# Kernel tuning notes

Hardware: AMD Instinct MI355X
Metric: run time of the kernel (lower is better)

Reference implementation:

```python
import jax, jax.numpy as jnp
import numpy as np

B, T, C, H = 4, 2048, 2048, 16
DH = C // H  # 128

def setup_inputs() -> dict:
    key = jax.random.key(0)
    ks = jax.random.split(key, 5)
    s_in = 1.0 / np.sqrt(C)
    return {
        "x": jax.random.normal(ks[0], (B, T, C), dtype=jnp.float32),
        "qkv_w": jax.random.uniform(ks[1], (3 * C, C), jnp.float32, -s_in, s_in),
        "qkv_b": jax.random.uniform(ks[2], (3 * C,), jnp.float32, -s_in, s_in),
        "proj_w": jax.random.uniform(ks[3], (C, C), jnp.float32, -s_in, s_in),
        "proj_b": jax.random.uniform(ks[4], (C,), jnp.float32, -s_in, s_in),
    }

def reference(x, qkv_w, qkv_b, proj_w, proj_b):
    b, t, _ = x.shape
    qkv = x @ qkv_w.T + qkv_b                     # [B,T,3C]
    q, k, v = jnp.split(qkv, 3, axis=-1)
    # [B,T,C] -> [B,H,T,Dh]
    q = q.reshape(b, t, H, DH).transpose(0, 2, 1, 3)
    k = k.reshape(b, t, H, DH).transpose(0, 2, 1, 3)
    v = v.reshape(b, t, H, DH).transpose(0, 2, 1, 3)
    scores = jnp.einsum('bhqd,bhkd->bhqk', q, k) / jnp.sqrt(jnp.float32(DH))
    causal = jnp.tril(jnp.ones((t, t), dtype=bool))  # [T,T]
    scores = jnp.where(causal[None, None], scores, jnp.finfo(scores.dtype).min)
    att = jax.nn.softmax(scores, axis=-1)
    out = jnp.einsum('bhqk,bhkd->bhqd', att, v)   # [B,H,T,Dh]
    out = out.transpose(0, 2, 1, 3).reshape(b, t, C)
    return out @ proj_w.T + proj_b
```

## Files before the change

kernel.cpp:

```cpp
#include <hip/hip_runtime.h>
#include <stdint.h>


typedef __attribute__((ext_vector_type(8))) short bf8_t;
typedef __attribute__((ext_vector_type(4))) float f4_t;

__device__ __forceinline__ short f2bf(float f) {
  union { float f; uint32_t u; } x; x.f = f;
  uint32_t r = x.u + 0x7fffu + ((x.u >> 16) & 1u);
  return (short)(r >> 16);
}

#define GLD16(gp, lp) __builtin_amdgcn_global_load_lds( \
    (const __attribute__((address_space(1))) void*)(gp), \
    (__attribute__((address_space(3))) void*)(lp), 16, 0, 0)

__device__ __forceinline__ bf8_t dsr(uint32_t a) {
  bf8_t d;
  asm volatile("ds_read_b128 %0, %1" : "=v"(d) : "v"(a));
  return d;
}

#define QSCALE (0.08838834764831845f * 1.4426950408889634f)

__global__ __launch_bounds__(256) void cast3_f32_bf16(
    const float* __restrict__ a, const float* __restrict__ b,
    const float* __restrict__ c, short* __restrict__ oa,
    short* __restrict__ ob, short* __restrict__ oc,
    int na4, int nb4, int nc4) {
  int i = blockIdx.x * blockDim.x + threadIdx.x;
  const float* src; short* dst; int idx;
  if (i < na4) { src = a; dst = oa; idx = i; }
  else if (i < na4 + nb4) { src = b; dst = ob; idx = i - na4; }
  else if (i < na4 + nb4 + nc4) { src = c; dst = oc; idx = i - na4 - nb4; }
  else return;
  float4 v = ((const float4*)src)[idx];
  short4 o;
  o.x = f2bf(v.x); o.y = f2bf(v.y); o.z = f2bf(v.z); o.w = f2bf(v.w);
  ((short4*)dst)[idx] = o;
}


#define BARR() do { __builtin_amdgcn_s_barrier(); \
                    __builtin_amdgcn_sched_barrier(0); } while (0)
#define WAITDS() do { asm volatile("s_waitcnt lgkmcnt(0)" ::: "memory"); \
                      __builtin_amdgcn_sched_barrier(0); } while (0)
#define SB() __builtin_amdgcn_sched_barrier(0)
#define PR1 __builtin_amdgcn_s_setprio(1)
#define PR0 __builtin_amdgcn_s_setprio(0)

#define STAGE(g, loff) do { \
    GLD16((g) + voff0, ldsc + (loff) + dst0); \
    GLD16((g) + voff1, ldsc + (loff) + 8192 + dst0); } while (0)

#define QUAD(CI, CJ, AF, BF)                                                \
  if (!swapAB) {                                                            \
    _Pragma("unroll") for (int kk = 0; kk < 2; ++kk)                        \
    _Pragma("unroll") for (int i = 0; i < 4; ++i)                           \
    _Pragma("unroll") for (int j = 0; j < 2; ++j)                           \
      acc[(CI) + i][(CJ) + j] = __builtin_amdgcn_mfma_f32_16x16x32_bf16(    \
          AF[i][kk], BF[j][kk], acc[(CI) + i][(CJ) + j], 0, 0, 0);          \
  } else {                                                                  \
    _Pragma("unroll") for (int kk = 0; kk < 2; ++kk)                        \
    _Pragma("unroll") for (int i = 0; i < 4; ++i)                           \
    _Pragma("unroll") for (int j = 0; j < 2; ++j)                           \
      acc[(CI) + i][(CJ) + j] = __builtin_amdgcn_mfma_f32_16x16x32_bf16(    \
          BF[j][kk], AF[i][kk], acc[(CI) + i][(CJ) + j], 0, 0, 0);          \
  }

template <int MODE>
__global__ __launch_bounds__(512, 2) void gemm_bt(
    const short* __restrict__ A, const short* __restrict__ Bw,
    const float* __restrict__ bias, float* __restrict__ Cout,
    short* __restrict__ Qo, short* __restrict__ Ko, short* __restrict__ Vo,
    int M, int N, int K) {
  __shared__ __attribute__((aligned(16))) char lds[131072];
  const int tid = threadIdx.x;
  const int lane = tid & 63, wave = tid >> 6;
  const int quad = lane >> 4, l16 = lane & 15;
  const int wm = wave >> 2, wn = wave & 3;

  const int nwg = gridDim.x;
  const int cpx = nwg >> 3;
  const int bid = blockIdx.x;
  const int swz = (bid & 7) * cpx + (bid >> 3);
  const int nbx = N >> 8;
  const int bm = swz / nbx, bn = swz - bm * nbx;
  const int m0 = bm << 8, n0 = bn << 8;

  const int which = (MODE == 0) ? (n0 >> 11) : -1;
  const bool swapAB = (MODE == 0) && (which == 2);


  f4_t acc[8][4];
  if (!swapAB) {
#pragma unroll
    for (int j = 0; j < 4; ++j) {
      const float b0 = bias[n0 + (j >> 1) * 128 + wn * 32 + (j & 1) * 16 + l16];
      const f4_t bv = {b0, b0, b0, b0};
#pragma unroll
      for (int i = 0; i < 8; ++i) acc[i][j] = bv;
    }
  } else {
#pragma unroll
    for (int j = 0; j < 4; ++j)
#pragma unroll
      for (int r = 0; r < 4; ++r) {
        const float b0 =
            bias[n0 + (j >> 1) * 128 + wn * 32 + (j & 1) * 16 + quad * 4 + r];
#pragma unroll
        for (int i = 0; i < 8; ++i) acc[i][j][r] = b0;
      }
  }

  const char* baseA = (const char*)(A + (size_t)m0 * K);
  const char* baseB = (const char*)(Bw + (size_t)n0 * K);
  const size_t hK = (size_t)K << 8;
  const int r0 = tid >> 3;
  const int lg = (tid & 7) ^ (r0 & 7);
  const uint32_t voff0 = (uint32_t)(r0 * K + lg * 8) * 2u;
  const uint32_t voff1 = voff0 + ((uint32_t)K << 7);
  char* ldsc = (char*)lds;
  const int dst0 = tid * 16;

  const int x7 = l16 & 7;
  const int gx0 = (quad ^ x7) << 4;
  const int gx1 = ((quad | 4) ^ x7) << 4;
  const uint32_t lbase =
      (uint32_t)(uintptr_t)(__attribute__((address_space(3))) char*)lds;
  const uint32_t aAg0 = lbase + wm * 8192 + l16 * 128 + gx0;
  const uint32_t aAg1 = lbase + wm * 8192 + l16 * 128 + gx1;
  const uint32_t bBg0 = lbase + 32768 + wn * 4096 + l16 * 128 + gx0;
  const uint32_t bBg1 = lbase + 32768 + wn * 4096 + l16 * 128 + gx1;

  asm volatile("s_waitcnt vmcnt(0)" ::: "memory");
  SB();

  STAGE(baseA, 0);
  STAGE(baseB, 32768);
  STAGE(baseB + hK, 49152);
  STAGE(baseA + hK, 16384);
  STAGE(baseA + 128, 65536 + 0);
  STAGE(baseB + hK + 128, 65536 + 49152);
  STAGE(baseA + hK + 128, 65536 + 16384);
  asm volatile("s_waitcnt vmcnt(6)" ::: "memory");
  SB();
  __builtin_amdgcn_s_barrier();

  const int NT = K >> 6;
  bf8_t af[4][2], b0f[2][2], b1f[2][2];

#pragma unroll
  for (int i = 0; i < 4; ++i) {
    af[i][0] = dsr(aAg0 + i * 2048);
    af[i][1] = dsr(aAg1 + i * 2048);
  }
#pragma unroll
  for (int j = 0; j < 2; ++j) {
    b0f[j][0] = dsr(bBg0 + j * 2048);
    b0f[j][1] = dsr(bBg1 + j * 2048);
  }

  for (int t = 0; t < NT; ++t) {
    const uint32_t s = (uint32_t)(t & 1) << 16;
    const uint32_t o = s ^ 65536u;
    const size_t c1 = (size_t)(t + 1 < NT ? t + 1 : NT - 1) << 7;
    const size_t c2 = (size_t)(t + 2 < NT ? t + 2 : NT - 1) << 7;
    const uint32_t sA0 = aAg0 + s, sA1 = aAg1 + s;
    const uint32_t sB0 = bBg0 + s, sB1 = bBg1 + s;

    WAITDS();
    STAGE(baseB + c1, (int)o + 32768);
    __builtin_amdgcn_s_barrier();
    SB();
    PR1; QUAD(0, 0, af, b0f); PR0;
    SB();
#pragma unroll
    for (int j = 0; j < 2; ++j) {
      b1f[j][0] = dsr(sB0 + 16384 + j * 2048);
      b1f[j][1] = dsr(sB1 + 16384 + j * 2048);
    }
    BARR();

    WAITDS();
    STAGE(baseA + c2, (int)s + 0);
    __builtin_amdgcn_s_barrier();
    SB();
    PR1; QUAD(0, 2, af, b1f); PR0;
    SB();
#pragma unroll
    for (int i = 0; i < 4; ++i) {
      af[i][0] = dsr(sA0 + 16384 + i * 2048);
      af[i][1] = dsr(sA1 + 16384 + i * 2048);
    }
    BARR();

    WAITDS();
    STAGE(baseB + hK + c2, (int)s + 49152);
    __builtin_amdgcn_s_barrier();
    SB();
    PR1; QUAD(4, 2, af, b1f); PR0;
    BARR();

    STAGE(baseA + hK + c2, (int)s + 16384);
    asm volatile("s_waitcnt vmcnt(6)" ::: "memory");
    SB();
    __builtin_amdgcn_s_barrier();
    SB();
    PR1; QUAD(4, 0, af, b0f); PR0;
    SB();
#pragma unroll
    for (int i = 0; i < 4; ++i) {
      af[i][0] = dsr(o + aAg0 + i * 2048);
      af[i][1] = dsr(o + aAg1 + i * 2048);
    }
#pragma unroll
    for (int j = 0; j < 2; ++j) {
      b0f[j][0] = dsr(o + bBg0 + j * 2048);
      b0f[j][1] = dsr(o + bBg1 + j * 2048);
    }
    BARR();
  }

  asm volatile("s_waitcnt vmcnt(0) lgkmcnt(0)" ::: "memory");
  SB();

  if (MODE == 1) {
#pragma unroll
    for (int i = 0; i < 8; ++i) {
      const int mg = m0 + (i >> 2) * 128 + wm * 64 + (i & 3) * 16 + quad * 4;
#pragma unroll
      for (int r = 0; r < 4; ++r) {
        const size_t mrow = (size_t)(mg + r) * N;
#pragma unroll
        for (int j = 0; j < 4; ++j) {
          const int ng = n0 + (j >> 1) * 128 + wn * 32 + (j & 1) * 16 + l16;
          Cout[mrow + ng] = acc[i][j][r];
        }
      }
    }
  } else if (!swapAB) {
    short* dst = (which == 0) ? Qo : Ko;
    const float sc = (which == 0) ? QSCALE : 1.0f;
#pragma unroll
    for (int i = 0; i < 8; ++i) {
      const int mg = m0 + (i >> 2) * 128 + wm * 64 + (i & 3) * 16 + quad * 4;
#pragma unroll
      for (int r = 0; r < 4; ++r) {
        const int m = mg + r;
        const int b = m >> 11, tt = m & 2047;
#pragma unroll
        for (int j = 0; j < 4; ++j) {
          const int ng = n0 + (j >> 1) * 128 + wn * 32 + (j & 1) * 16 + l16;
          const int h = (ng & 2047) >> 7, d = ng & 127;
          dst[((size_t)((b * 16 + h) * 2048 + tt)) * 128 + d] =
              f2bf(acc[i][j][r] * sc);
        }
      }
    }
  } else {
#pragma unroll
    for (int i = 0; i < 8; ++i) {
      const int mg = m0 + (i >> 2) * 128 + wm * 64 + (i & 3) * 16 + l16;
      const int b = mg >> 11, tt = mg & 2047;
#pragma unroll
      for (int j = 0; j < 4; ++j) {
        const int nb = n0 + (j >> 1) * 128 + wn * 32 + (j & 1) * 16 + quad * 4;
#pragma unroll
        for (int r = 0; r < 4; ++r) {
          const int ng = nb + r;
          const int h = (ng & 2047) >> 7, d = ng & 127;
          Vo[((size_t)((b * 16 + h) * 128 + d)) * 2048 + tt] =
              f2bf(acc[i][j][r]);
        }
      }
    }
  }
}

__global__ __launch_bounds__(256) void attn_fwd(
    const short* __restrict__ Qg, const short* __restrict__ Kg,
    const short* __restrict__ Vtg, short* __restrict__ Og) {
  __shared__ __attribute__((aligned(16))) short lK[64 * 128];
  __shared__ __attribute__((aligned(16))) short lV[128 * 64];
  __shared__ __attribute__((aligned(16))) short lP[4 * 2048];
  const int tid = threadIdx.x;
  const int lane = tid & 63, wave = tid >> 6;
  const int quad = lane >> 4, l16 = lane & 15;
  const int bid = blockIdx.x;
  const int bh = ((bid & 7) << 3) | ((bid >> 3) & 7);
  const int p = bid >> 6;
  const size_t baseK = (size_t)bh * (2048 * 128);
  const size_t baseV = (size_t)bh * (128 * 2048);
  const int x7 = l16 & 7;
  const int b = bh >> 4, h = bh & 15;
  short* lPw = lP + wave * 2048;
  const f4_t fz = {0.f, 0.f, 0.f, 0.f};

  uint32_t vK[4], vV[4];
#pragma unroll
  for (int r = 0; r < 4; ++r) {
    const int off = tid * 16 + r * 4096;
    const int rowK = off >> 8;
    const int lcK = ((off >> 4) & 15) ^ (rowK & 7);
    vK[r] = (uint32_t)(rowK * 128 + lcK * 8) * 2u;
    const int dV = off >> 7;
    const int lcV = ((off >> 4) & 7) ^ (dV & 7);
    vV[r] = (uint32_t)(dV * 2048 + lcV * 8) * 2u;
  }

  for (int job = 0; job < 2; ++job) {
    const int bx = job ? (15 - p) : p;
    const int q0 = bx * 128;
    const int qw = q0 + wave * 32;

    bf8_t qf[2][4];
#pragma unroll
    for (int m = 0; m < 2; ++m)
#pragma unroll
      for (int dc = 0; dc < 4; ++dc)
        qf[m][dc] = *(const bf8_t*)(Qg + baseK + (size_t)(qw + m * 16 + l16) * 128 + dc * 32 + quad * 8);

    f4_t o[2][8];
#pragma unroll
    for (int m = 0; m < 2; ++m)
#pragma unroll
      for (int n = 0; n < 8; ++n) o[m][n] = fz;
    float lsum[2][4];
#pragma unroll
    for (int m = 0; m < 2; ++m)
#pragma unroll
      for (int r = 0; r < 4; ++r) lsum[m][r] = 0.f;

    const char* kbase = (const char*)(Kg + baseK);
    const char* vbase = (const char*)(Vtg + baseV);
    const int ktmax = 2 * bx + 1;
    for (int kt = 0; kt <= ktmax; ++kt) {
      const int k0 = kt * 64;
      __syncthreads();
#pragma unroll
      for (int r = 0; r < 4; ++r) {
        const int off = tid * 16 + r * 4096;
        GLD16(kbase + vK[r], (char*)lK + off);
        GLD16(vbase + vV[r], (char*)lV + off);
      }
      kbase += 16384;
      vbase += 128;
      __syncthreads();
      if (k0 >= qw + 32) continue;

      f4_t s[2][4];
#pragma unroll
      for (int m = 0; m < 2; ++m)
#pragma unroll
        for (int g = 0; g < 4; ++g) s[m][g] = fz;
#pragma unroll
      for (int g = 0; g < 4; ++g)
#pragma unroll
        for (int dc = 0; dc < 4; ++dc) {
          bf8_t kf = *(const bf8_t*)(lK + (g * 16 + l16) * 128 + (((dc * 4 + quad) ^ x7) << 3));
          s[0][g] = __builtin_amdgcn_mfma_f32_16x16x32_bf16(qf[0][dc], kf, s[0][g], 0, 0, 0);
          s[1][g] = __builtin_amdgcn_mfma_f32_16x16x32_bf16(qf[1][dc], kf, s[1][g], 0, 0, 0);
        }
#pragma unroll
      for (int m = 0; m < 2; ++m) {
        const int qbase = qw + m * 16;
        const bool nomask = (k0 + 63 <= qbase);
#pragma unroll
        for (int g = 0; g < 4; ++g) {
          const int key = k0 + g * 16 + l16;
#pragma unroll
          for (int r = 0; r < 4; ++r) {
            float pv = exp2f(s[m][g][r]);
            if (!nomask && key > qbase + quad * 4 + r) pv = 0.f;
            lsum[m][r] += pv;
            const int row = quad * 4 + r;
            lPw[m * 1024 + row * 64 + (((g * 2 + (l16 >> 3)) ^ (row & 7)) << 3) + x7] = f2bf(pv);
          }
        }
      }
      bf8_t pa[2][2];
#pragma unroll
      for (int m = 0; m < 2; ++m)
#pragma unroll
        for (int kc = 0; kc < 2; ++kc)
          pa[m][kc] = *(const bf8_t*)(lPw + m * 1024 + l16 * 64 + (((kc * 4 + quad) ^ x7) << 3));
#pragma unroll
      for (int n = 0; n < 8; ++n)
#pragma unroll
        for (int kc = 0; kc < 2; ++kc) {
          bf8_t vf = *(const bf8_t*)(lV + (n * 16 + l16) * 64 + (((kc * 4 + quad) ^ x7) << 3));
          o[0][n] = __builtin_amdgcn_mfma_f32_16x16x32_bf16(pa[0][kc], vf, o[0][n], 0, 0, 0);
          o[1][n] = __builtin_amdgcn_mfma_f32_16x16x32_bf16(pa[1][kc], vf, o[1][n], 0, 0, 0);
        }
    }
#pragma unroll
    for (int m = 0; m < 2; ++m)
#pragma unroll
      for (int r = 0; r < 4; ++r) {
        float v = lsum[m][r];
        v += __shfl_xor(v, 1, 64);
        v += __shfl_xor(v, 2, 64);
        v += __shfl_xor(v, 4, 64);
        v += __shfl_xor(v, 8, 64);
        const float inv = 1.f / v;
        const int t = qw + m * 16 + quad * 4 + r;
        const size_t orow = ((size_t)(b * 2048 + t)) * 2048 + h * 128;
#pragma unroll
        for (int n = 0; n < 8; ++n)
          Og[orow + n * 16 + l16] = f2bf(o[m][n][r] * inv);
      }
  }
}

extern "C" void kernel_launch(void* const* d_in, const int* in_sizes, int n_in,
                              void* d_out, int out_size, void* d_ws, size_t ws_size,
                              hipStream_t stream) {
  const float* x      = (const float*)d_in[0];
  const float* qkv_w  = (const float*)d_in[1];
  const float* qkv_b  = (const float*)d_in[2];
  const float* proj_w = (const float*)d_in[3];
  const float* proj_b = (const float*)d_in[4];
  float* out = (float*)d_out;

  char* ws = (char*)d_ws;
  short* xb    = (short*)(ws);
  short* wqkv  = (short*)(ws + 33554432);
  short* wproj = (short*)(ws + 58720256);
  short* qb    = (short*)(ws + 67108864);
  short* kb    = (short*)(ws + 100663296);
  short* vb    = (short*)(ws + 134217728);
  short* attb  = (short*)(ws + 167772160);

  cast3_f32_bf16<<<32768, 256, 0, stream>>>(x, qkv_w, proj_w, xb, wqkv, wproj,
                                            4194304, 3145728, 1048576);

  gemm_bt<0><<<768, 512, 0, stream>>>(xb, wqkv, qkv_b, nullptr,
                                      qb, kb, vb, 8192, 6144, 2048);
  attn_fwd<<<512, 256, 0, stream>>>(qb, kb, vb, attb);
  gemm_bt<1><<<256, 512, 0, stream>>>(attb, wproj, proj_b, out,
                                      nullptr, nullptr, nullptr, 8192, 2048, 2048);
}
```

Baseline: 589.6 us.

## Load K/V fragments directly from global memory in attention, dropping LDS staging

The attention kernel no longer stages K and V tiles in shared memory with block-wide barriers. Each wave reads its MFMA operands straight from global memory (relying on L2/L1 caching) and runs its own per-wave key-loop bound, so it skips tiles past its causal limit without waiting on other waves. This removes two syncthreads per tile and the LDS traffic, but each wave now fetches K/V redundantly from cache, with less coalesced 16-byte loads and no latency hiding from staging.

```diff
diff --git a/kernel.cpp b/kernel.cpp
--- a/kernel.cpp
+++ b/kernel.cpp
@@ -91,7 +91,6 @@
   const int which = (MODE == 0) ? (n0 >> 11) : -1;
   const bool swapAB = (MODE == 0) && (which == 2);
 
-
   f4_t acc[8][4];
   if (!swapAB) {
 #pragma unroll
@@ -281,8 +280,6 @@
 __global__ __launch_bounds__(256) void attn_fwd(
     const short* __restrict__ Qg, const short* __restrict__ Kg,
     const short* __restrict__ Vtg, short* __restrict__ Og) {
-  __shared__ __attribute__((aligned(16))) short lK[64 * 128];
-  __shared__ __attribute__((aligned(16))) short lV[128 * 64];
   __shared__ __attribute__((aligned(16))) short lP[4 * 2048];
   const int tid = threadIdx.x;
   const int lane = tid & 63, wave = tid >> 6;
@@ -297,18 +294,6 @@
   short* lPw = lP + wave * 2048;
   const f4_t fz = {0.f, 0.f, 0.f, 0.f};
 
-  uint32_t vK[4], vV[4];
-#pragma unroll
-  for (int r = 0; r < 4; ++r) {
-    const int off = tid * 16 + r * 4096;
-    const int rowK = off >> 8;
-    const int lcK = ((off >> 4) & 15) ^ (rowK & 7);
-    vK[r] = (uint32_t)(rowK * 128 + lcK * 8) * 2u;
-    const int dV = off >> 7;
-    const int lcV = ((off >> 4) & 7) ^ (dV & 7);
-    vV[r] = (uint32_t)(dV * 2048 + lcV * 8) * 2u;
-  }
-
   for (int job = 0; job < 2; ++job) {
     const int bx = job ? (15 - p) : p;
     const int q0 = bx * 128;
@@ -332,22 +317,11 @@
 #pragma unroll
       for (int r = 0; r < 4; ++r) lsum[m][r] = 0.f;
 
-    const char* kbase = (const char*)(Kg + baseK);
-    const char* vbase = (const char*)(Vtg + baseV);
-    const int ktmax = 2 * bx + 1;
-    for (int kt = 0; kt <= ktmax; ++kt) {
+    const short* Kb = Kg + baseK;
+    const short* Vb = Vtg + baseV;
+    const int ktend = (qw + 95) >> 6;
+    for (int kt = 0; kt < ktend; ++kt) {
       const int k0 = kt * 64;
-      __syncthreads();
-#pragma unroll
-      for (int r = 0; r < 4; ++r) {
-        const int off = tid * 16 + r * 4096;
-        GLD16(kbase + vK[r], (char*)lK + off);
-        GLD16(vbase + vV[r], (char*)lV + off);
-      }
-      kbase += 16384;
-      vbase += 128;
-      __syncthreads();
-      if (k0 >= qw + 32) continue;
 
       f4_t s[2][4];
 #pragma unroll
@@ -355,13 +329,15 @@
 #pragma unroll
         for (int g = 0; g < 4; ++g) s[m][g] = fz;
 #pragma unroll
-      for (int g = 0; g < 4; ++g)
+      for (int g = 0; g < 4; ++g) {
+        const short* krow = Kb + (size_t)(k0 + g * 16 + l16) * 128 + quad * 8;
 #pragma unroll
         for (int dc = 0; dc < 4; ++dc) {
-          bf8_t kf = *(const bf8_t*)(lK + (g * 16 + l16) * 128 + (((dc * 4 + quad) ^ x7) << 3));
+          bf8_t kf = *(const bf8_t*)(krow + dc * 32);
           s[0][g] = __builtin_amdgcn_mfma_f32_16x16x32_bf16(qf[0][dc], kf, s[0][g], 0, 0, 0);
           s[1][g] = __builtin_amdgcn_mfma_f32_16x16x32_bf16(qf[1][dc], kf, s[1][g], 0, 0, 0);
         }
+      }
 #pragma unroll
       for (int m = 0; m < 2; ++m) {
         const int qbase = qw + m * 16;
@@ -386,13 +362,15 @@
         for (int kc = 0; kc < 2; ++kc)
           pa[m][kc] = *(const bf8_t*)(lPw + m * 1024 + l16 * 64 + (((kc * 4 + quad) ^ x7) << 3));
 #pragma unroll
-      for (int n = 0; n < 8; ++n)
+      for (int n = 0; n < 8; ++n) {
+        const short* vrow = Vb + (size_t)(n * 16 + l16) * 2048 + k0 + quad * 8;
 #pragma unroll
         for (int kc = 0; kc < 2; ++kc) {
-          bf8_t vf = *(const bf8_t*)(lV + (n * 16 + l16) * 64 + (((kc * 4 + quad) ^ x7) << 3));
+          bf8_t vf = *(const bf8_t*)(vrow + kc * 32);
           o[0][n] = __builtin_amdgcn_mfma_f32_16x16x32_bf16(pa[0][kc], vf, o[0][n], 0, 0, 0);
           o[1][n] = __builtin_amdgcn_mfma_f32_16x16x32_bf16(pa[1][kc], vf, o[1][n], 0, 0, 0);
         }
+      }
     }
 #pragma unroll
     for (int m = 0; m < 2; ++m)
```

Result: slower. 736.4 us (+24.9%).

## Double-buffer K/V tiles in attention and pipeline LDS fragment reads

Applied to the files above, without the earlier changes.

The attention kernel now keeps two LDS buffers for the K and V tiles and prefetches the next tile with global_load_lds while the current one is computed. This replaces the two barriers per iteration with one barrier plus a vmcnt wait. K and V fragments are read with inline ds_read asm, double-buffered in registers, and waited on with explicit lgkmcnt counts so the LDS reads overlap the MFMA work. LDS use grows to 80KB per block, which may lower occupancy, and the hand-written waitcnt counts make the code fragile.

```diff
diff --git a/kernel.cpp b/kernel.cpp
--- a/kernel.cpp
+++ b/kernel.cpp
@@ -19,6 +19,9 @@
   bf8_t d;
   asm volatile("ds_read_b128 %0, %1" : "=v"(d) : "v"(a));
   return d;
+}
+__device__ __forceinline__ void dsw16(uint32_t a, uint32_t v) {
+  asm volatile("ds_write_b16 %0, %1" :: "v"(a), "v"(v));
 }
 
 #define QSCALE (0.08838834764831845f * 1.4426950408889634f)
@@ -91,7 +94,6 @@
   const int which = (MODE == 0) ? (n0 >> 11) : -1;
   const bool swapAB = (MODE == 0) && (which == 2);
 
-
   f4_t acc[8][4];
   if (!swapAB) {
 #pragma unroll
@@ -281,21 +283,25 @@
 __global__ __launch_bounds__(256) void attn_fwd(
     const short* __restrict__ Qg, const short* __restrict__ Kg,
     const short* __restrict__ Vtg, short* __restrict__ Og) {
-  __shared__ __attribute__((aligned(16))) short lK[64 * 128];
-  __shared__ __attribute__((aligned(16))) short lV[128 * 64];
-  __shared__ __attribute__((aligned(16))) short lP[4 * 2048];
+  __shared__ __attribute__((aligned(16))) char ldsA[81920];
   const int tid = threadIdx.x;
   const int lane = tid & 63, wave = tid >> 6;
   const int quad = lane >> 4, l16 = lane & 15;
   const int bid = blockIdx.x;
   const int bh = ((bid & 7) << 3) | ((bid >> 3) & 7);
   const int p = bid >> 6;
-  const size_t baseK = (size_t)bh * (2048 * 128);
-  const size_t baseV = (size_t)bh * (128 * 2048);
+  const size_t baseK0 = (size_t)bh * (2048 * 128);
+  const size_t baseV0 = (size_t)bh * (128 * 2048);
   const int x7 = l16 & 7;
   const int b = bh >> 4, h = bh & 15;
-  short* lPw = lP + wave * 2048;
+  char* ldsc = (char*)ldsA;
   const f4_t fz = {0.f, 0.f, 0.f, 0.f};
+
+  const uint32_t lbase =
+      (uint32_t)(uintptr_t)(__attribute__((address_space(3))) char*)ldsA;
+  const uint32_t kRow = lbase + (uint32_t)l16 * 256;
+  const uint32_t vRow = lbase + 32768u + (uint32_t)l16 * 128;
+  const uint32_t pB = lbase + 65536u + (uint32_t)wave * 4096;
 
   uint32_t vK[4], vV[4];
 #pragma unroll
@@ -319,7 +325,7 @@
     for (int m = 0; m < 2; ++m)
 #pragma unroll
       for (int dc = 0; dc < 4; ++dc)
-        qf[m][dc] = *(const bf8_t*)(Qg + baseK + (size_t)(qw + m * 16 + l16) * 128 + dc * 32 + quad * 8);
+        qf[m][dc] = *(const bf8_t*)(Qg + baseK0 + (size_t)(qw + m * 16 + l16) * 128 + dc * 32 + quad * 8);
 
     f4_t o[2][8];
 #pragma unroll
@@ -332,67 +338,119 @@
 #pragma unroll
       for (int r = 0; r < 4; ++r) lsum[m][r] = 0.f;
 
-    const char* kbase = (const char*)(Kg + baseK);
-    const char* vbase = (const char*)(Vtg + baseV);
+    const char* kbase = (const char*)(Kg + baseK0);
+    const char* vbase = (const char*)(Vtg + baseV0);
     const int ktmax = 2 * bx + 1;
+
+#pragma unroll
+    for (int r = 0; r < 4; ++r) {
+      GLD16(kbase + vK[r], ldsc + tid * 16 + r * 4096);
+      GLD16(vbase + vV[r], ldsc + 32768 + tid * 16 + r * 4096);
+    }
+    kbase += 16384; vbase += 128;
+    asm volatile("s_waitcnt vmcnt(0)" ::: "memory");
+    SB();
+    __builtin_amdgcn_s_barrier();
+    SB();
+
     for (int kt = 0; kt <= ktmax; ++kt) {
       const int k0 = kt * 64;
-      __syncthreads();
-#pragma unroll
-      for (int r = 0; r < 4; ++r) {
-        const int off = tid * 16 + r * 4096;
-        GLD16(kbase + vK[r], (char*)lK + off);
-        GLD16(vbase + vV[r], (char*)lV + off);
-      }
-      kbase += 16384;
-      vbase += 128;
-      __syncthreads();
-      if (k0 >= qw + 32) continue;
-
-      f4_t s[2][4];
-#pragma unroll
-      for (int m = 0; m < 2; ++m)
-#pragma unroll
-        for (int g = 0; g < 4; ++g) s[m][g] = fz;
-#pragma unroll
-      for (int g = 0; g < 4; ++g)
-#pragma unroll
-        for (int dc = 0; dc < 4; ++dc) {
-          bf8_t kf = *(const bf8_t*)(lK + (g * 16 + l16) * 128 + (((dc * 4 + quad) ^ x7) << 3));
-          s[0][g] = __builtin_amdgcn_mfma_f32_16x16x32_bf16(qf[0][dc], kf, s[0][g], 0, 0, 0);
-          s[1][g] = __builtin_amdgcn_mfma_f32_16x16x32_bf16(qf[1][dc], kf, s[1][g], 0, 0, 0);
-        }
-#pragma unroll
-      for (int m = 0; m < 2; ++m) {
-        const int qbase = qw + m * 16;
-        const bool nomask = (k0 + 63 <= qbase);
+      const uint32_t cb = (uint32_t)(kt & 1) << 14;
+      const uint32_t nb = cb ^ 16384u;
+
+      if (kt < ktmax) {
+#pragma unroll
+        for (int r = 0; r < 4; ++r) {
+          GLD16(kbase + vK[r], ldsc + nb + tid * 16 + r * 4096);
+          GLD16(vbase + vV[r], ldsc + 32768 + nb + tid * 16 + r * 4096);
+        }
+        kbase += 16384; vbase += 128;
+      }
+      SB();
+
+      if (k0 < qw + 32) {
+        f4_t s[2][4];
+#pragma unroll
+        for (int m = 0; m < 2; ++m)
+#pragma unroll
+          for (int g = 0; g < 4; ++g) s[m][g] = fz;
+        const uint32_t kB = kRow + cb;
+        bf8_t kf[2][4];
+#pragma unroll
+        for (int dc = 0; dc < 4; ++dc)
+          kf[0][dc] = dsr(kB + (uint32_t)((((dc * 4 + quad) ^ x7) << 4)));
 #pragma unroll
         for (int g = 0; g < 4; ++g) {
-          const int key = k0 + g * 16 + l16;
-#pragma unroll
-          for (int r = 0; r < 4; ++r) {
-            float pv = exp2f(s[m][g][r]);
-            if (!nomask && key > qbase + quad * 4 + r) pv = 0.f;
-            lsum[m][r] += pv;
-            const int row = quad * 4 + r;
-            lPw[m * 1024 + row * 64 + (((g * 2 + (l16 >> 3)) ^ (row & 7)) << 3) + x7] = f2bf(pv);
+          const int cs = g & 1, ns2 = cs ^ 1;
+          if (g < 3) {
+#pragma unroll
+            for (int dc = 0; dc < 4; ++dc)
+              kf[ns2][dc] = dsr(kB + (uint32_t)((g + 1) * 4096 + (((dc * 4 + quad) ^ x7) << 4)));
+            asm volatile("s_waitcnt lgkmcnt(4)" ::: "memory");
+            SB();
+          } else {
+            asm volatile("s_waitcnt lgkmcnt(0)" ::: "memory");
+            SB();
           }
-        }
-      }
-      bf8_t pa[2][2];
-#pragma unroll
-      for (int m = 0; m < 2; ++m)
+#pragma unroll
+          for (int dc = 0; dc < 4; ++dc) {
+            s[0][g] = __builtin_amdgcn_mfma_f32_16x16x32_bf16(qf[0][dc], kf[cs][dc], s[0][g], 0, 0, 0);
+            s[1][g] = __builtin_amdgcn_mfma_f32_16x16x32_bf16(qf[1][dc], kf[cs][dc], s[1][g], 0, 0, 0);
+          }
+        }
+#pragma unroll
+        for (int m = 0; m < 2; ++m) {
+          const int qbase = qw + m * 16;
+          const bool nomask = (k0 + 63 <= qbase);
+#pragma unroll
+          for (int g = 0; g < 4; ++g) {
+            const int key = k0 + g * 16 + l16;
+#pragma unroll
+            for (int r = 0; r < 4; ++r) {
+              float pv = exp2f(s[m][g][r]);
+              if (!nomask && key > qbase + quad * 4 + r) pv = 0.f;
+              lsum[m][r] += pv;
+              const int row = quad * 4 + r;
+              const uint32_t wa = pB + (uint32_t)(m * 2048 + row * 128 +
+                  ((((g * 2 + (l16 >> 3)) ^ (row & 7)) << 4)) + x7 * 2);
+              dsw16(wa, (uint32_t)(uint16_t)f2bf(pv));
+            }
+          }
+        }
+        const uint32_t vB = vRow + cb;
+        bf8_t pa[2][2], vf[2][2];
+#pragma unroll
+        for (int m = 0; m < 2; ++m)
+#pragma unroll
+          for (int kc = 0; kc < 2; ++kc)
+            pa[m][kc] = dsr(pB + (uint32_t)(m * 2048 + l16 * 128 + (((kc * 4 + quad) ^ x7) << 4)));
 #pragma unroll
         for (int kc = 0; kc < 2; ++kc)
-          pa[m][kc] = *(const bf8_t*)(lPw + m * 1024 + l16 * 64 + (((kc * 4 + quad) ^ x7) << 3));
-#pragma unroll
-      for (int n = 0; n < 8; ++n)
-#pragma unroll
-        for (int kc = 0; kc < 2; ++kc) {
-          bf8_t vf = *(const bf8_t*)(lV + (n * 16 + l16) * 64 + (((kc * 4 + quad) ^ x7) << 3));
-          o[0][n] = __builtin_amdgcn_mfma_f32_16x16x32_bf16(pa[0][kc], vf, o[0][n], 0, 0, 0);
-          o[1][n] = __builtin_amdgcn_mfma_f32_16x16x32_bf16(pa[1][kc], vf, o[1][n], 0, 0, 0);
-        }
+          vf[0][kc] = dsr(vB + (uint32_t)(((kc * 4 + quad) ^ x7) << 4));
+#pragma unroll
+        for (int n = 0; n < 8; ++n) {
+          const int cs = n & 1, ns2 = cs ^ 1;
+          if (n < 7) {
+#pragma unroll
+            for (int kc = 0; kc < 2; ++kc)
+              vf[ns2][kc] = dsr(vB + (uint32_t)((n + 1) * 2048 + (((kc * 4 + quad) ^ x7) << 4)));
+            asm volatile("s_waitcnt lgkmcnt(2)" ::: "memory");
+            SB();
+          } else {
+            asm volatile("s_waitcnt lgkmcnt(0)" ::: "memory");
+            SB();
+          }
+#pragma unroll
+          for (int kc = 0; kc < 2; ++kc) {
+            o[0][n] = __builtin_amdgcn_mfma_f32_16x16x32_bf16(pa[0][kc], vf[cs][kc], o[0][n], 0, 0, 0);
+            o[1][n] = __builtin_amdgcn_mfma_f32_16x16x32_bf16(pa[1][kc], vf[cs][kc], o[1][n], 0, 0, 0);
+          }
+        }
+      }
+      asm volatile("s_waitcnt vmcnt(0)" ::: "memory");
+      SB();
+      __builtin_amdgcn_s_barrier();
+      SB();
     }
 #pragma unroll
     for (int m = 0; m < 2; ++m)
```

Result: slower. 611.2 us (+3.7%).

## Compute transposed attention scores and pack P writes; grid-stride cast kernel

Applied to the files above, without the earlier changes.

The QK^T MFMA is issued with swapped operands so each lane holds four consecutive keys for a single query row. That lets the probabilities be packed with v_cvt_pk_bf16_f32 and written to LDS as one ds_write_b64 instead of many scalar short stores. The row sum becomes one scalar per lane, reduced across quads at the end and broadcast per row with a shuffle. Separately, the cast kernel becomes a grid-stride loop launched with far fewer blocks. The trade-off is an explicit lgkmcnt wait plus inline asm, and the correctness of the swizzled P layout must match the read path.

```diff
diff --git a/kernel.cpp b/kernel.cpp
--- a/kernel.cpp
+++ b/kernel.cpp
@@ -4,6 +4,7 @@
 
 typedef __attribute__((ext_vector_type(8))) short bf8_t;
 typedef __attribute__((ext_vector_type(4))) float f4_t;
+typedef __attribute__((ext_vector_type(2))) unsigned int u2_t;
 
 __device__ __forceinline__ short f2bf(float f) {
   union { float f; uint32_t u; } x; x.f = f;
@@ -28,16 +29,18 @@
     const float* __restrict__ c, short* __restrict__ oa,
     short* __restrict__ ob, short* __restrict__ oc,
     int na4, int nb4, int nc4) {
-  int i = blockIdx.x * blockDim.x + threadIdx.x;
-  const float* src; short* dst; int idx;
-  if (i < na4) { src = a; dst = oa; idx = i; }
-  else if (i < na4 + nb4) { src = b; dst = ob; idx = i - na4; }
-  else if (i < na4 + nb4 + nc4) { src = c; dst = oc; idx = i - na4 - nb4; }
-  else return;
-  float4 v = ((const float4*)src)[idx];
-  short4 o;
-  o.x = f2bf(v.x); o.y = f2bf(v.y); o.z = f2bf(v.z); o.w = f2bf(v.w);
-  ((short4*)dst)[idx] = o;
+  const int total = na4 + nb4 + nc4;
+  const int stride = gridDim.x * blockDim.x;
+  for (int i = blockIdx.x * blockDim.x + threadIdx.x; i < total; i += stride) {
+    const float* src; short* dst; int idx;
+    if (i < na4) { src = a; dst = oa; idx = i; }
+    else if (i < na4 + nb4) { src = b; dst = ob; idx = i - na4; }
+    else { src = c; dst = oc; idx = i - na4 - nb4; }
+    float4 v = ((const float4*)src)[idx];
+    short4 o;
+    o.x = f2bf(v.x); o.y = f2bf(v.y); o.z = f2bf(v.z); o.w = f2bf(v.w);
+    ((short4*)dst)[idx] = o;
+  }
 }
 
 
@@ -90,7 +93,6 @@
 
   const int which = (MODE == 0) ? (n0 >> 11) : -1;
   const bool swapAB = (MODE == 0) && (which == 2);
-
 
   f4_t acc[8][4];
   if (!swapAB) {
@@ -295,6 +297,9 @@
   const int x7 = l16 & 7;
   const int b = bh >> 4, h = bh & 15;
   short* lPw = lP + wave * 2048;
+  const uint32_t pBw =
+      (uint32_t)(uintptr_t)(__attribute__((address_space(3))) short*)lP +
+      (uint32_t)wave * 4096u;
   const f4_t fz = {0.f, 0.f, 0.f, 0.f};
 
   uint32_t vK[4], vV[4];
@@ -326,11 +331,8 @@
     for (int m = 0; m < 2; ++m)
 #pragma unroll
       for (int n = 0; n < 8; ++n) o[m][n] = fz;
-    float lsum[2][4];
-#pragma unroll
-    for (int m = 0; m < 2; ++m)
-#pragma unroll
-      for (int r = 0; r < 4; ++r) lsum[m][r] = 0.f;
+    float lsum[2];
+    lsum[0] = 0.f; lsum[1] = 0.f;
 
     const char* kbase = (const char*)(Kg + baseK);
     const char* vbase = (const char*)(Vtg + baseV);
@@ -349,36 +351,49 @@
       __syncthreads();
       if (k0 >= qw + 32) continue;
 
-      f4_t s[2][4];
+      f4_t st[2][4];
 #pragma unroll
       for (int m = 0; m < 2; ++m)
 #pragma unroll
-        for (int g = 0; g < 4; ++g) s[m][g] = fz;
+        for (int g = 0; g < 4; ++g) st[m][g] = fz;
 #pragma unroll
       for (int g = 0; g < 4; ++g)
 #pragma unroll
         for (int dc = 0; dc < 4; ++dc) {
           bf8_t kf = *(const bf8_t*)(lK + (g * 16 + l16) * 128 + (((dc * 4 + quad) ^ x7) << 3));
-          s[0][g] = __builtin_amdgcn_mfma_f32_16x16x32_bf16(qf[0][dc], kf, s[0][g], 0, 0, 0);
-          s[1][g] = __builtin_amdgcn_mfma_f32_16x16x32_bf16(qf[1][dc], kf, s[1][g], 0, 0, 0);
+          st[0][g] = __builtin_amdgcn_mfma_f32_16x16x32_bf16(kf, qf[0][dc], st[0][g], 0, 0, 0);
+          st[1][g] = __builtin_amdgcn_mfma_f32_16x16x32_bf16(kf, qf[1][dc], st[1][g], 0, 0, 0);
         }
 #pragma unroll
       for (int m = 0; m < 2; ++m) {
         const int qbase = qw + m * 16;
+        const int qv = qbase + l16;
         const bool nomask = (k0 + 63 <= qbase);
 #pragma unroll
         for (int g = 0; g < 4; ++g) {
-          const int key = k0 + g * 16 + l16;
-#pragma unroll
-          for (int r = 0; r < 4; ++r) {
-            float pv = exp2f(s[m][g][r]);
-            if (!nomask && key > qbase + quad * 4 + r) pv = 0.f;
-            lsum[m][r] += pv;
-            const int row = quad * 4 + r;
-            lPw[m * 1024 + row * 64 + (((g * 2 + (l16 >> 3)) ^ (row & 7)) << 3) + x7] = f2bf(pv);
+          const int kb2 = k0 + g * 16 + quad * 4;
+          float pv0 = exp2f(st[m][g][0]);
+          float pv1 = exp2f(st[m][g][1]);
+          float pv2 = exp2f(st[m][g][2]);
+          float pv3 = exp2f(st[m][g][3]);
+          if (!nomask) {
+            if (kb2 + 0 > qv) pv0 = 0.f;
+            if (kb2 + 1 > qv) pv1 = 0.f;
+            if (kb2 + 2 > qv) pv2 = 0.f;
+            if (kb2 + 3 > qv) pv3 = 0.f;
           }
-        }
-      }
+          lsum[m] += (pv0 + pv1) + (pv2 + pv3);
+          uint32_t w01, w23;
+          asm("v_cvt_pk_bf16_f32 %0, %1, %2" : "=v"(w01) : "v"(pv0), "v"(pv1));
+          asm("v_cvt_pk_bf16_f32 %0, %1, %2" : "=v"(w23) : "v"(pv2), "v"(pv3));
+          u2_t wv; wv.x = w01; wv.y = w23;
+          const uint32_t wa = pBw + (uint32_t)(m * 2048 + l16 * 128 +
+              ((((g * 2 + (quad >> 1)) ^ x7)) << 4) + (quad & 1) * 8);
+          asm volatile("ds_write_b64 %0, %1" :: "v"(wa), "v"(wv) : "memory");
+        }
+      }
+      asm volatile("s_waitcnt lgkmcnt(0)" ::: "memory");
+      SB();
       bf8_t pa[2][2];
 #pragma unroll
       for (int m = 0; m < 2; ++m)
@@ -394,16 +409,19 @@
           o[1][n] = __builtin_amdgcn_mfma_f32_16x16x32_bf16(pa[1][kc], vf, o[1][n], 0, 0, 0);
         }
     }
+    float tot[2];
+#pragma unroll
+    for (int m = 0; m < 2; ++m) {
+      float v = lsum[m];
+      v += __shfl_xor(v, 16, 64);
+      v += __shfl_xor(v, 32, 64);
+      tot[m] = v;
+    }
 #pragma unroll
     for (int m = 0; m < 2; ++m)
 #pragma unroll
       for (int r = 0; r < 4; ++r) {
-        float v = lsum[m][r];
-        v += __shfl_xor(v, 1, 64);
-        v += __shfl_xor(v, 2, 64);
-        v += __shfl_xor(v, 4, 64);
-        v += __shfl_xor(v, 8, 64);
-        const float inv = 1.f / v;
+        const float inv = 1.f / __shfl(tot[m], quad * 4 + r, 16);
         const int t = qw + m * 16 + quad * 4 + r;
         const size_t orow = ((size_t)(b * 2048 + t)) * 2048 + h * 128;
 #pragma unroll
@@ -432,8 +450,8 @@
   short* vb    = (short*)(ws + 134217728);
   short* attb  = (short*)(ws + 167772160);
 
-  cast3_f32_bf16<<<32768, 256, 0, stream>>>(x, qkv_w, proj_w, xb, wqkv, wproj,
-                                            4194304, 3145728, 1048576);
+  cast3_f32_bf16<<<2048, 256, 0, stream>>>(x, qkv_w, proj_w, xb, wqkv, wproj,
+                                           4194304, 3145728, 1048576);
 
   gemm_bt<0><<<768, 512, 0, stream>>>(xb, wqkv, qkv_b, nullptr,
                                       qb, kb, vb, 8192, 6144, 2048);
```

After: 582.6 us. Within noise of the previous version (-1.2%).
